# Optimization experiments

Hardware: AMD Instinct MI355X
Metric: run time of the kernel (lower is better)

The kernel has to match this reference:

```python
import jax, jax.numpy as jnp
import numpy as np

N = 8192
E = 262144
IN_F = 256
OUT_F = 64
H = 2
SLOPE = 0.2
NEG = -9e15


def _xavier(key, shape, gain):
    fan_in, fan_out = shape[-2], shape[-1]
    a = gain * np.sqrt(6.0 / (fan_in + fan_out))
    return jax.random.uniform(key, shape, jnp.float32, -a, a)


def setup_inputs() -> dict:
    key = jax.random.key(0)
    k_x, k_e, k_w, k_a1, k_a2 = jax.random.split(key, 5)
    gain = np.sqrt(2.0)
    return {
        "x": jax.random.normal(k_x, (N, IN_F), jnp.float32),
        "edge_index": jax.random.randint(k_e, (2, E), 0, N, jnp.int64),
        # per-head params (torch Linear stores weight [out,in]; we store [in,out])
        "W": _xavier(k_w, (H, IN_F, OUT_F), gain),
        "a1": _xavier(k_a1, (H, OUT_F), gain),
        "a2": _xavier(k_a2, (H, OUT_F), gain),
    }


def reference(x, edge_index, W, a1, a2):
    n = x.shape[0]
    # dense adjacency mask from COO edges (to_dense_adj: adj[src, dst] += 1; only adj>0 matters)
    adj = jnp.zeros((n, n), jnp.float32).at[edge_index[0], edge_index[1]].add(1.0)
    mask = adj > 0  # [N, N]

    xh = jnp.einsum('ni,hio->hno', x, W)          # [H, N, out]
    s1 = jnp.einsum('hno,ho->hn', xh, a1)          # a1(x): [H, N]
    s2 = jnp.einsum('hno,ho->hn', xh, a2)          # a2(x): [H, N]
    e = jnp.where(mask[None], s1[:, :, None] + s2[:, None, :], NEG)  # [H, N, N]
    e = jnp.where(e >= 0, e, SLOPE * e)            # leaky_relu
    att = jax.nn.softmax(e, axis=-1)               # [H, N, N]
    out = jnp.einsum('hnm,hmo->hno', att, xh)      # [H, N, out]
    # concat heads along feature dim (is_final_layer=False)
    return jnp.transpose(out, (1, 0, 2)).reshape(n, H * OUT_F)
```

## Files before the change

kernel.cpp:

```cpp
#include <hip/hip_runtime.h>

#define NN    8192
#define INF_  256
#define OUTF  64
#define NH    2
#define NE    262144
#define CAP   256
#define DEGS  16
#define SLOPE 0.2f

typedef __attribute__((ext_vector_type(8))) short short8;
typedef __attribute__((ext_vector_type(4))) float f32x4;
typedef __attribute__((ext_vector_type(2))) long long ll2;

__device__ __forceinline__ unsigned short f2bf(float f) {
  unsigned int u = __float_as_uint(f);
  u += 0x7fffu + ((u >> 16) & 1u);
  return (unsigned short)(u >> 16);
}

__global__ __launch_bounds__(256) void gemm_edge_kernel(
    const float* __restrict__ x, const int* __restrict__ ei,
    const float* __restrict__ W, const float* __restrict__ a1,
    const float* __restrict__ a2, int* __restrict__ deg,
    int* __restrict__ cols, float* __restrict__ xh,
    float2* __restrict__ s1v, float2* __restrict__ s2v) {
  const int b = blockIdx.x, t = threadIdx.x;

  __shared__ int s_nz;
  if (t == 0) s_nz = 0;
  __syncthreads();
  const int e0 = b * 512 + t * 2;
  if (((const unsigned int*)ei)[2 * e0 + 1] != 0u ||
      ((const unsigned int*)ei)[2 * e0 + 3] != 0u)
    s_nz = 1;
  __syncthreads();

  int i0, j0, i1, j1;
  if (s_nz == 0) {
    const ll2 a = *(const ll2*)((const long long*)ei + e0);
    const ll2 c = *(const ll2*)((const long long*)ei + NE + e0);
    i0 = (int)a[0]; i1 = (int)a[1]; j0 = (int)c[0]; j1 = (int)c[1];
  } else {
    const int2 a = *(const int2*)(ei + e0);
    const int2 c = *(const int2*)(ei + NE + e0);
    i0 = a.x; i1 = a.y; j0 = c.x; j1 = c.y;
  }
  const int p0 = atomicAdd(&deg[i0 * DEGS], 1);
  const int p1 = atomicAdd(&deg[i1 * DEGS], 1);

  const int l = t & 63, w = t >> 6;
  const int lo = l & 15, hi = l >> 4;
  const int n0 = b * 16;
  __shared__ float p1s[4][16], p2s[4][16];

  const int tc0 = w * 2, tc1 = w * 2 + 1;
  const int h0 = tc0 >> 2, h1 = tc1 >> 2;
  const int col0 = (tc0 * 16 + lo) & 63, col1 = (tc1 * 16 + lo) & 63;
  const float* wp0 = W + (size_t)h0 * (INF_ * OUTF) + (size_t)(hi * 8) * OUTF + col0;
  const float* wp1 = W + (size_t)h1 * (INF_ * OUTF) + (size_t)(hi * 8) * OUTF + col1;
  const float* xp = x + (size_t)(n0 + lo) * INF_ + hi * 8;

  f32x4 acc0 = {0.f, 0.f, 0.f, 0.f};
  f32x4 acc1 = {0.f, 0.f, 0.f, 0.f};

#define KSTEP(ks)                                                              \
  {                                                                            \
    const float4 f0 = *(const float4*)(xp + (ks) * 32);                        \
    const float4 f1 = *(const float4*)(xp + (ks) * 32 + 4);                    \
    short8 a_;                                                                 \
    a_[0] = (short)f2bf(f0.x); a_[1] = (short)f2bf(f0.y);                      \
    a_[2] = (short)f2bf(f0.z); a_[3] = (short)f2bf(f0.w);                      \
    a_[4] = (short)f2bf(f1.x); a_[5] = (short)f2bf(f1.y);                      \
    a_[6] = (short)f2bf(f1.z); a_[7] = (short)f2bf(f1.w);                      \
    const float* wq0 = wp0 + (size_t)(ks) * 32 * OUTF;                         \
    short8 b0_;                                                                \
    b0_[0] = (short)f2bf(wq0[0 * OUTF]); b0_[1] = (short)f2bf(wq0[1 * OUTF]);  \
    b0_[2] = (short)f2bf(wq0[2 * OUTF]); b0_[3] = (short)f2bf(wq0[3 * OUTF]);  \
    b0_[4] = (short)f2bf(wq0[4 * OUTF]); b0_[5] = (short)f2bf(wq0[5 * OUTF]);  \
    b0_[6] = (short)f2bf(wq0[6 * OUTF]); b0_[7] = (short)f2bf(wq0[7 * OUTF]);  \
    acc0 = __builtin_amdgcn_mfma_f32_16x16x32_bf16(a_, b0_, acc0, 0, 0, 0);    \
    const float* wq1 = wp1 + (size_t)(ks) * 32 * OUTF;                         \
    short8 b1_;                                                                \
    b1_[0] = (short)f2bf(wq1[0 * OUTF]); b1_[1] = (short)f2bf(wq1[1 * OUTF]);  \
    b1_[2] = (short)f2bf(wq1[2 * OUTF]); b1_[3] = (short)f2bf(wq1[3 * OUTF]);  \
    b1_[4] = (short)f2bf(wq1[4 * OUTF]); b1_[5] = (short)f2bf(wq1[5 * OUTF]);  \
    b1_[6] = (short)f2bf(wq1[6 * OUTF]); b1_[7] = (short)f2bf(wq1[7 * OUTF]);  \
    acc1 = __builtin_amdgcn_mfma_f32_16x16x32_bf16(a_, b1_, acc1, 0, 0, 0);    \
  }

  KSTEP(0) KSTEP(1) KSTEP(2) KSTEP(3) KSTEP(4) KSTEP(5) KSTEP(6) KSTEP(7)
#undef KSTEP

  if (p0 < CAP) cols[i0 * CAP + p0] = j0;
  if (p1 < CAP) cols[i1 * CAP + p1] = j1;

  {
    float* o0 = xh + ((size_t)h0 * NN + n0 + hi * 4) * OUTF + col0;
    float* o1 = xh + ((size_t)h1 * NN + n0 + hi * 4) * OUTF + col1;
    o0[0 * OUTF] = acc0[0]; o0[1 * OUTF] = acc0[1];
    o0[2 * OUTF] = acc0[2]; o0[3 * OUTF] = acc0[3];
    o1[0 * OUTF] = acc1[0]; o1[1 * OUTF] = acc1[1];
    o1[2 * OUTF] = acc1[2]; o1[3 * OUTF] = acc1[3];
  }
  const float a10 = a1[h0 * OUTF + col0], a11 = a1[h1 * OUTF + col1];
  const float a20 = a2[h0 * OUTF + col0], a21 = a2[h1 * OUTF + col1];
#pragma unroll
  for (int r = 0; r < 4; ++r) {
    float p1v = acc0[r] * a10 + acc1[r] * a11;
    float p2v = acc0[r] * a20 + acc1[r] * a21;
#pragma unroll
    for (int s = 1; s < 16; s <<= 1) {
      p1v += __shfl_xor(p1v, s, 64);
      p2v += __shfl_xor(p2v, s, 64);
    }
    if (lo == 0) {
      p1s[w][hi * 4 + r] = p1v;
      p2s[w][hi * 4 + r] = p2v;
    }
  }
  __syncthreads();
  if (t < 16) {
    float2 v1, v2;
    v1.x = p1s[0][t] + p1s[1][t];  v1.y = p1s[2][t] + p1s[3][t];
    v2.x = p2s[0][t] + p2s[1][t];  v2.y = p2s[2][t] + p2s[3][t];
    s1v[n0 + t] = v1;
    s2v[n0 + t] = v2;
  }
}

__global__ __launch_bounds__(128) void agg_kernel(const float* __restrict__ xh,
                                                  const float2* __restrict__ s1v,
                                                  const float2* __restrict__ s2v,
                                                  const int* __restrict__ deg,
                                                  const int* __restrict__ cols,
                                                  float* __restrict__ out) {
  const int i = blockIdx.x;
  const int t = threadIdx.x;
  const int h = t >> 6, lane = t & 63;
  __shared__ unsigned int bm[NN / 32];
  __shared__ unsigned long long vmask;
  __shared__ int   cjs[CAP];
  __shared__ float wts[NH][CAP];
  int d = deg[i * DEGS];
  if (d > CAP) d = CAP;
  bm[t] = 0u; bm[t + 128] = 0u;
  __syncthreads();

  const float* base = xh + (size_t)h * NN * OUTF;
  const int c4 = lane & 15, r = lane >> 4;

  if (d == 0) {
    f32x4 acc = {0.f, 0.f, 0.f, 0.f};
    for (int p = r; p < NN; p += 4)
      acc += *(const f32x4*)(base + (size_t)p * OUTF + 4 * c4);
#pragma unroll
    for (int c = 0; c < 4; ++c) {
      acc[c] += __shfl_xor(acc[c], 16, 64);
      acc[c] += __shfl_xor(acc[c], 32, 64);
    }
    if (lane < 16) {
      const float sc = 1.f / (float)NN;
      float4 o;
      o.x = acc[0] * sc; o.y = acc[1] * sc; o.z = acc[2] * sc; o.w = acc[3] * sc;
      *(float4*)(out + (size_t)i * (NH * OUTF) + h * OUTF + 4 * lane) = o;
    }
    return;
  }

  if (d <= 64) {
    int j = 0;
    const bool valid = lane < d;
    if (valid) j = cols[i * CAP + lane];
    if (h == 0) {
      bool dup = false;
      if (valid) {
        const unsigned int old = atomicOr(&bm[j >> 5], 1u << (j & 31));
        dup = (old >> (j & 31)) & 1u;
      }
      const unsigned long long bal = __ballot(valid && !dup);
      if (lane == 0) vmask = bal;
    }
    __syncthreads();
    const bool kp = (vmask >> lane) & 1ull;
    float sc = -1e30f;
    if (kp) {
      const float2 s1i2 = s1v[i];
      const float2 s2j2 = s2v[j];
      sc = (h ? s1i2.y : s1i2.x) + (h ? s2j2.y : s2j2.x);
      sc = (sc >= 0.f) ? sc : SLOPE * sc;
    }
    float m = sc;
#pragma unroll
    for (int s = 32; s > 0; s >>= 1) m = fmaxf(m, __shfl_xor(m, s, 64));
    const float wt = kp ? __expf(sc - m) : 0.f;
    float ds = wt;
#pragma unroll
    for (int s = 32; s > 0; s >>= 1) ds += __shfl_xor(ds, s, 64);
    const float inv = 1.f / ds;

    f32x4 acc = {0.f, 0.f, 0.f, 0.f};
#pragma unroll 2
    for (int p = 0; p < d; p += 4) {
      const int pr = p + r;
      float ww = __shfl(wt, pr, 64);
      int   jj = __shfl(j,  pr, 64);
      ww = (pr < d) ? ww : 0.f;
      jj = (ww > 0.f) ? jj : 0;
      acc += ww * *(const f32x4*)(base + (size_t)jj * OUTF + 4 * c4);
    }
#pragma unroll
    for (int c = 0; c < 4; ++c) {
      acc[c] += __shfl_xor(acc[c], 16, 64);
      acc[c] += __shfl_xor(acc[c], 32, 64);
    }
    if (lane < 16) {
      float4 o;
      o.x = acc[0] * inv; o.y = acc[1] * inv; o.z = acc[2] * inv; o.w = acc[3] * inv;
      *(float4*)(out + (size_t)i * (NH * OUTF) + h * OUTF + 4 * lane) = o;
    }
    return;
  }

  for (int p = t; p < d; p += 128) cjs[p] = cols[i * CAP + p];
  __syncthreads();
  if (h == 0) {
    for (int p = lane; p < d; p += 64) {
      const int j = cjs[p];
      const unsigned int old = atomicOr(&bm[j >> 5], 1u << (j & 31));
      if ((old >> (j & 31)) & 1u) cjs[p] = -1;
    }
  }
  __syncthreads();
  const float2 s1i2 = s1v[i];
  const float s1i = h ? s1i2.y : s1i2.x;
  float m = -1e30f;
  for (int p = lane; p < d; p += 64) {
    const int j = cjs[p];
    float sc = -1e30f;
    if (j >= 0) {
      const float2 s2j2 = s2v[j];
      sc = s1i + (h ? s2j2.y : s2j2.x);
      sc = (sc >= 0.f) ? sc : SLOPE * sc;
    }
    wts[h][p] = sc;
    m = fmaxf(m, sc);
  }
#pragma unroll
  for (int s = 32; s > 0; s >>= 1) m = fmaxf(m, __shfl_xor(m, s, 64));
  float ds = 0.f;
  for (int p = lane; p < d; p += 64) {
    const float sc = wts[h][p];
    const float w2 = (sc > -1e29f) ? __expf(sc - m) : 0.f;
    wts[h][p] = w2;
    ds += w2;
  }
#pragma unroll
  for (int s = 32; s > 0; s >>= 1) ds += __shfl_xor(ds, s, 64);
  const float inv = 1.f / ds;
  float acc = 0.f;
  for (int p = 0; p < d; ++p) {
    const float w2 = wts[h][p];
    if (w2 > 0.f) acc += w2 * base[(size_t)cjs[p] * OUTF + lane];
  }
  out[(size_t)i * (NH * OUTF) + h * OUTF + lane] = acc * inv;
}

extern "C" void kernel_launch(void* const* d_in, const int* in_sizes, int n_in,
                              void* d_out, int out_size, void* d_ws, size_t ws_size,
                              hipStream_t stream) {
  const float* x  = (const float*)d_in[0];
  const int*   ei = (const int*)d_in[1];
  const float* W  = (const float*)d_in[2];
  const float* a1 = (const float*)d_in[3];
  const float* a2 = (const float*)d_in[4];
  float* out = (float*)d_out;

  char* ws = (char*)d_ws;
  float*  xh   = (float*)(ws);
  float2* s1v  = (float2*)(ws + (4u << 20));
  float2* s2v  = (float2*)(ws + (4u << 20) + (64u << 10));
  int*    deg  = (int*)  (ws + (4u << 20) + (128u << 10));
  int*    cols = (int*)  (ws + (5u << 20));

  hipMemsetAsync(deg, 0, (size_t)NN * DEGS * 4, stream);
  gemm_edge_kernel<<<512, 256, 0, stream>>>(x, ei, W, a1, a2, deg, cols,
                                            xh, s1v, s2v);
  agg_kernel<<<NN, 128, 0, stream>>>(xh, s1v, s2v, deg, cols, out);
}
```

Baseline: 48.64 us.

## Split degree counters into four sub-buckets and separate edge blocks from GEMM blocks

Edge insertion now runs in its own 512 blocks, launched alongside the GEMM blocks instead of inside them. Each node's adjacency list is split into four sub-buckets of 64 slots, selected by edge index mod 4, which spreads atomic contention across four padded counters. The aggregation kernel reads the four counts, builds prefix offsets and remaps each slot index to its sub-bucket. This costs a 4x larger memset, extra branching in agg, and a lower per-bucket capacity that could drop edges when a bucket holds more than 64.

```diff
diff --git a/kernel.cpp b/kernel.cpp
--- a/kernel.cpp
+++ b/kernel.cpp
@@ -1,13 +1,15 @@
 #include <hip/hip_runtime.h>
 
-#define NN    8192
-#define INF_  256
-#define OUTF  64
-#define NH    2
-#define NE    262144
-#define CAP   256
-#define DEGS  16
-#define SLOPE 0.2f
+#define NN     8192
+#define INF_   256
+#define OUTF   64
+#define NH     2
+#define NE     262144
+#define CAP    256
+#define NSUB   4
+#define SUBCAP 64
+#define DEGS   16
+#define SLOPE  0.2f
 
 typedef __attribute__((ext_vector_type(8))) short short8;
 typedef __attribute__((ext_vector_type(4))) float f32x4;
@@ -27,27 +29,33 @@
     float2* __restrict__ s1v, float2* __restrict__ s2v) {
   const int b = blockIdx.x, t = threadIdx.x;
 
-  __shared__ int s_nz;
-  if (t == 0) s_nz = 0;
-  __syncthreads();
-  const int e0 = b * 512 + t * 2;
-  if (((const unsigned int*)ei)[2 * e0 + 1] != 0u ||
-      ((const unsigned int*)ei)[2 * e0 + 3] != 0u)
-    s_nz = 1;
-  __syncthreads();
-
-  int i0, j0, i1, j1;
-  if (s_nz == 0) {
-    const ll2 a = *(const ll2*)((const long long*)ei + e0);
-    const ll2 c = *(const ll2*)((const long long*)ei + NE + e0);
-    i0 = (int)a[0]; i1 = (int)a[1]; j0 = (int)c[0]; j1 = (int)c[1];
-  } else {
-    const int2 a = *(const int2*)(ei + e0);
-    const int2 c = *(const int2*)(ei + NE + e0);
-    i0 = a.x; i1 = a.y; j0 = c.x; j1 = c.y;
-  }
-  const int p0 = atomicAdd(&deg[i0 * DEGS], 1);
-  const int p1 = atomicAdd(&deg[i1 * DEGS], 1);
+  if (b >= 512) {
+    const int eb = b - 512;
+    const int e0 = eb * 512 + t * 2;
+    __shared__ int s_nz;
+    if (t == 0) s_nz = 0;
+    __syncthreads();
+    if (((const unsigned int*)ei)[2 * e0 + 1] != 0u ||
+        ((const unsigned int*)ei)[2 * e0 + 3] != 0u)
+      s_nz = 1;
+    __syncthreads();
+    int i0, j0, i1, j1;
+    if (s_nz == 0) {
+      const ll2 a = *(const ll2*)((const long long*)ei + e0);
+      const ll2 c = *(const ll2*)((const long long*)ei + NE + e0);
+      i0 = (int)a[0]; i1 = (int)a[1]; j0 = (int)c[0]; j1 = (int)c[1];
+    } else {
+      const int2 a = *(const int2*)(ei + e0);
+      const int2 c = *(const int2*)(ei + NE + e0);
+      i0 = a.x; i1 = a.y; j0 = c.x; j1 = c.y;
+    }
+    const int c0 = e0 & 3, c1 = (e0 + 1) & 3;
+    const int p0 = atomicAdd(&deg[(c0 * NN + i0) * DEGS], 1);
+    if (p0 < SUBCAP) cols[i0 * CAP + c0 * SUBCAP + p0] = j0;
+    const int p1 = atomicAdd(&deg[(c1 * NN + i1) * DEGS], 1);
+    if (p1 < SUBCAP) cols[i1 * CAP + c1 * SUBCAP + p1] = j1;
+    return;
+  }
 
   const int l = t & 63, w = t >> 6;
   const int lo = l & 15, hi = l >> 4;
@@ -92,9 +100,6 @@
   KSTEP(0) KSTEP(1) KSTEP(2) KSTEP(3) KSTEP(4) KSTEP(5) KSTEP(6) KSTEP(7)
 #undef KSTEP
 
-  if (p0 < CAP) cols[i0 * CAP + p0] = j0;
-  if (p1 < CAP) cols[i1 * CAP + p1] = j1;
-
   {
     float* o0 = xh + ((size_t)h0 * NN + n0 + hi * 4) * OUTF + col0;
     float* o1 = xh + ((size_t)h1 * NN + n0 + hi * 4) * OUTF + col1;
@@ -142,8 +147,16 @@
   __shared__ unsigned long long vmask;
   __shared__ int   cjs[CAP];
   __shared__ float wts[NH][CAP];
-  int d = deg[i * DEGS];
-  if (d > CAP) d = CAP;
+
+  int cnt0 = deg[(0 * NN + i) * DEGS];
+  int cnt1 = deg[(1 * NN + i) * DEGS];
+  int cnt2 = deg[(2 * NN + i) * DEGS];
+  int cnt3 = deg[(3 * NN + i) * DEGS];
+  cnt0 = min(cnt0, SUBCAP); cnt1 = min(cnt1, SUBCAP);
+  cnt2 = min(cnt2, SUBCAP); cnt3 = min(cnt3, SUBCAP);
+  const int P1 = cnt0, P2 = P1 + cnt1, P3 = P2 + cnt2;
+  const int d = __builtin_amdgcn_readfirstlane(P3 + cnt3);
+
   bm[t] = 0u; bm[t + 128] = 0u;
   __syncthreads();
 
@@ -171,7 +184,14 @@
   if (d <= 64) {
     int j = 0;
     const bool valid = lane < d;
-    if (valid) j = cols[i * CAP + lane];
+    if (valid) {
+      int cc, off;
+      if (lane < P1)      { cc = 0; off = lane; }
+      else if (lane < P2) { cc = 1; off = lane - P1; }
+      else if (lane < P3) { cc = 2; off = lane - P2; }
+      else                { cc = 3; off = lane - P3; }
+      j = cols[i * CAP + cc * SUBCAP + off];
+    }
     if (h == 0) {
       bool dup = false;
       if (valid) {
@@ -222,7 +242,14 @@
     return;
   }
 
-  for (int p = t; p < d; p += 128) cjs[p] = cols[i * CAP + p];
+  for (int p = t; p < d; p += 128) {
+    int cc, off;
+    if (p < P1)      { cc = 0; off = p; }
+    else if (p < P2) { cc = 1; off = p - P1; }
+    else if (p < P3) { cc = 2; off = p - P2; }
+    else             { cc = 3; off = p - P3; }
+    cjs[p] = cols[i * CAP + cc * SUBCAP + off];
+  }
   __syncthreads();
   if (h == 0) {
     for (int p = lane; p < d; p += 64) {
@@ -281,10 +308,10 @@
   float2* s1v  = (float2*)(ws + (4u << 20));
   float2* s2v  = (float2*)(ws + (4u << 20) + (64u << 10));
   int*    deg  = (int*)  (ws + (4u << 20) + (128u << 10));
-  int*    cols = (int*)  (ws + (5u << 20));
-
-  hipMemsetAsync(deg, 0, (size_t)NN * DEGS * 4, stream);
-  gemm_edge_kernel<<<512, 256, 0, stream>>>(x, ei, W, a1, a2, deg, cols,
-                                            xh, s1v, s2v);
+  int*    cols = (int*)  (ws + (7u << 20));
+
+  hipMemsetAsync(deg, 0, (size_t)NSUB * NN * DEGS * 4, stream);
+  gemm_edge_kernel<<<1024, 256, 0, stream>>>(x, ei, W, a1, a2, deg, cols,
+                                             xh, s1v, s2v);
   agg_kernel<<<NN, 128, 0, stream>>>(xh, s1v, s2v, deg, cols, out);
 }
```

Result: faster. 46.54 us (-4.3%).

## Replace CSR edge lists with dense adjacency bitmap and in-kernel compaction

Applied to the files above, without the earlier changes.

Edges are now recorded by atomicOr into a per-row 8192-bit bitmap, which replaces the per-row degree counters and column lists. The edge pass moves into separate blocks of the first kernel, so GEMM blocks no longer carry edge work. The aggregation kernel rebuilds a deduplicated, sorted neighbor list with popcount plus a wave prefix scan, which removes the shared-memory duplicate detection and the conditional branches. In exchange, an 8 MB bitmap must be zeroed by memset and read once per row, adding memory traffic compared with the old small degree and column arrays.

```diff
diff --git a/kernel.cpp b/kernel.cpp
--- a/kernel.cpp
+++ b/kernel.cpp
@@ -5,8 +5,7 @@
 #define OUTF  64
 #define NH    2
 #define NE    262144
-#define CAP   256
-#define DEGS  16
+#define NW    256
 #define SLOPE 0.2f
 
 typedef __attribute__((ext_vector_type(8))) short short8;
@@ -22,32 +21,35 @@
 __global__ __launch_bounds__(256) void gemm_edge_kernel(
     const float* __restrict__ x, const int* __restrict__ ei,
     const float* __restrict__ W, const float* __restrict__ a1,
-    const float* __restrict__ a2, int* __restrict__ deg,
-    int* __restrict__ cols, float* __restrict__ xh,
-    float2* __restrict__ s1v, float2* __restrict__ s2v) {
+    const float* __restrict__ a2, unsigned* __restrict__ bits,
+    float* __restrict__ xh, float2* __restrict__ s1v,
+    float2* __restrict__ s2v) {
   const int b = blockIdx.x, t = threadIdx.x;
 
-  __shared__ int s_nz;
-  if (t == 0) s_nz = 0;
-  __syncthreads();
-  const int e0 = b * 512 + t * 2;
-  if (((const unsigned int*)ei)[2 * e0 + 1] != 0u ||
-      ((const unsigned int*)ei)[2 * e0 + 3] != 0u)
-    s_nz = 1;
-  __syncthreads();
-
-  int i0, j0, i1, j1;
-  if (s_nz == 0) {
-    const ll2 a = *(const ll2*)((const long long*)ei + e0);
-    const ll2 c = *(const ll2*)((const long long*)ei + NE + e0);
-    i0 = (int)a[0]; i1 = (int)a[1]; j0 = (int)c[0]; j1 = (int)c[1];
-  } else {
-    const int2 a = *(const int2*)(ei + e0);
-    const int2 c = *(const int2*)(ei + NE + e0);
-    i0 = a.x; i1 = a.y; j0 = c.x; j1 = c.y;
-  }
-  const int p0 = atomicAdd(&deg[i0 * DEGS], 1);
-  const int p1 = atomicAdd(&deg[i1 * DEGS], 1);
+  if (b >= 512) {
+    const int eb = b - 512;
+    const int e0 = eb * 512 + t * 2;
+    __shared__ int s_nz;
+    if (t == 0) s_nz = 0;
+    __syncthreads();
+    if (((const unsigned int*)ei)[2 * e0 + 1] != 0u ||
+        ((const unsigned int*)ei)[2 * e0 + 3] != 0u)
+      s_nz = 1;
+    __syncthreads();
+    int i0, j0, i1, j1;
+    if (s_nz == 0) {
+      const ll2 a = *(const ll2*)((const long long*)ei + e0);
+      const ll2 c = *(const ll2*)((const long long*)ei + NE + e0);
+      i0 = (int)a[0]; i1 = (int)a[1]; j0 = (int)c[0]; j1 = (int)c[1];
+    } else {
+      const int2 a = *(const int2*)(ei + e0);
+      const int2 c = *(const int2*)(ei + NE + e0);
+      i0 = a.x; i1 = a.y; j0 = c.x; j1 = c.y;
+    }
+    atomicOr(&bits[(size_t)i0 * NW + (j0 >> 5)], 1u << (j0 & 31));
+    atomicOr(&bits[(size_t)i1 * NW + (j1 >> 5)], 1u << (j1 & 31));
+    return;
+  }
 
   const int l = t & 63, w = t >> 6;
   const int lo = l & 15, hi = l >> 4;
@@ -92,9 +94,6 @@
   KSTEP(0) KSTEP(1) KSTEP(2) KSTEP(3) KSTEP(4) KSTEP(5) KSTEP(6) KSTEP(7)
 #undef KSTEP
 
-  if (p0 < CAP) cols[i0 * CAP + p0] = j0;
-  if (p1 < CAP) cols[i1 * CAP + p1] = j1;
-
   {
     float* o0 = xh + ((size_t)h0 * NN + n0 + hi * 4) * OUTF + col0;
     float* o1 = xh + ((size_t)h1 * NN + n0 + hi * 4) * OUTF + col1;
@@ -132,19 +131,36 @@
 __global__ __launch_bounds__(128) void agg_kernel(const float* __restrict__ xh,
                                                   const float2* __restrict__ s1v,
                                                   const float2* __restrict__ s2v,
-                                                  const int* __restrict__ deg,
-                                                  const int* __restrict__ cols,
+                                                  const unsigned* __restrict__ bits,
                                                   float* __restrict__ out) {
   const int i = blockIdx.x;
   const int t = threadIdx.x;
   const int h = t >> 6, lane = t & 63;
-  __shared__ unsigned int bm[NN / 32];
-  __shared__ unsigned long long vmask;
-  __shared__ int   cjs[CAP];
-  __shared__ float wts[NH][CAP];
-  int d = deg[i * DEGS];
-  if (d > CAP) d = CAP;
-  bm[t] = 0u; bm[t + 128] = 0u;
+  __shared__ int   cjs[NH][256];
+  __shared__ float wts[NH][256];
+
+  const uint4 bv = *(const uint4*)(bits + (size_t)i * NW + lane * 4);
+  const int myc = __popc(bv.x) + __popc(bv.y) + __popc(bv.z) + __popc(bv.w);
+  int incl = myc;
+#pragma unroll
+  for (int s = 1; s < 64; s <<= 1) {
+    const int v = __shfl_up(incl, s, 64);
+    if (lane >= s) incl += v;
+  }
+  int pos = incl - myc;
+  const int dt = __shfl(incl, 63, 64);
+  const int d = __builtin_amdgcn_readfirstlane(dt > 256 ? 256 : dt);
+  {
+    unsigned wv; int bj;
+    wv = bv.x; bj = lane * 128;
+    while (wv) { const int bb = __ffs(wv) - 1; if (pos < 256) cjs[h][pos] = bj + bb; ++pos; wv &= wv - 1; }
+    wv = bv.y; bj = lane * 128 + 32;
+    while (wv) { const int bb = __ffs(wv) - 1; if (pos < 256) cjs[h][pos] = bj + bb; ++pos; wv &= wv - 1; }
+    wv = bv.z; bj = lane * 128 + 64;
+    while (wv) { const int bb = __ffs(wv) - 1; if (pos < 256) cjs[h][pos] = bj + bb; ++pos; wv &= wv - 1; }
+    wv = bv.w; bj = lane * 128 + 96;
+    while (wv) { const int bb = __ffs(wv) - 1; if (pos < 256) cjs[h][pos] = bj + bb; ++pos; wv &= wv - 1; }
+  }
   __syncthreads();
 
   const float* base = xh + (size_t)h * NN * OUTF;
@@ -169,20 +185,8 @@
   }
 
   if (d <= 64) {
-    int j = 0;
-    const bool valid = lane < d;
-    if (valid) j = cols[i * CAP + lane];
-    if (h == 0) {
-      bool dup = false;
-      if (valid) {
-        const unsigned int old = atomicOr(&bm[j >> 5], 1u << (j & 31));
-        dup = (old >> (j & 31)) & 1u;
-      }
-      const unsigned long long bal = __ballot(valid && !dup);
-      if (lane == 0) vmask = bal;
-    }
-    __syncthreads();
-    const bool kp = (vmask >> lane) & 1ull;
+    const bool kp = lane < d;
+    const int j = kp ? cjs[h][lane] : 0;
     float sc = -1e30f;
     if (kp) {
       const float2 s1i2 = s1v[i];
@@ -222,27 +226,13 @@
     return;
   }
 
-  for (int p = t; p < d; p += 128) cjs[p] = cols[i * CAP + p];
-  __syncthreads();
-  if (h == 0) {
-    for (int p = lane; p < d; p += 64) {
-      const int j = cjs[p];
-      const unsigned int old = atomicOr(&bm[j >> 5], 1u << (j & 31));
-      if ((old >> (j & 31)) & 1u) cjs[p] = -1;
-    }
-  }
-  __syncthreads();
   const float2 s1i2 = s1v[i];
   const float s1i = h ? s1i2.y : s1i2.x;
   float m = -1e30f;
   for (int p = lane; p < d; p += 64) {
-    const int j = cjs[p];
-    float sc = -1e30f;
-    if (j >= 0) {
-      const float2 s2j2 = s2v[j];
-      sc = s1i + (h ? s2j2.y : s2j2.x);
-      sc = (sc >= 0.f) ? sc : SLOPE * sc;
-    }
+    const float2 s2j2 = s2v[cjs[h][p]];
+    float sc = s1i + (h ? s2j2.y : s2j2.x);
+    sc = (sc >= 0.f) ? sc : SLOPE * sc;
     wts[h][p] = sc;
     m = fmaxf(m, sc);
   }
@@ -250,8 +240,7 @@
   for (int s = 32; s > 0; s >>= 1) m = fmaxf(m, __shfl_xor(m, s, 64));
   float ds = 0.f;
   for (int p = lane; p < d; p += 64) {
-    const float sc = wts[h][p];
-    const float w2 = (sc > -1e29f) ? __expf(sc - m) : 0.f;
+    const float w2 = __expf(wts[h][p] - m);
     wts[h][p] = w2;
     ds += w2;
   }
@@ -259,10 +248,8 @@
   for (int s = 32; s > 0; s >>= 1) ds += __shfl_xor(ds, s, 64);
   const float inv = 1.f / ds;
   float acc = 0.f;
-  for (int p = 0; p < d; ++p) {
-    const float w2 = wts[h][p];
-    if (w2 > 0.f) acc += w2 * base[(size_t)cjs[p] * OUTF + lane];
-  }
+  for (int p = 0; p < d; ++p)
+    acc += wts[h][p] * base[(size_t)cjs[h][p] * OUTF + lane];
   out[(size_t)i * (NH * OUTF) + h * OUTF + lane] = acc * inv;
 }
 
@@ -277,14 +264,13 @@
   float* out = (float*)d_out;
 
   char* ws = (char*)d_ws;
-  float*  xh   = (float*)(ws);
-  float2* s1v  = (float2*)(ws + (4u << 20));
-  float2* s2v  = (float2*)(ws + (4u << 20) + (64u << 10));
-  int*    deg  = (int*)  (ws + (4u << 20) + (128u << 10));
-  int*    cols = (int*)  (ws + (5u << 20));
-
-  hipMemsetAsync(deg, 0, (size_t)NN * DEGS * 4, stream);
-  gemm_edge_kernel<<<512, 256, 0, stream>>>(x, ei, W, a1, a2, deg, cols,
-                                            xh, s1v, s2v);
-  agg_kernel<<<NN, 128, 0, stream>>>(xh, s1v, s2v, deg, cols, out);
-}
+  unsigned* bits = (unsigned*)(ws);
+  float*    xh   = (float*)(ws + (8u << 20));
+  float2*   s1v  = (float2*)(ws + (12u << 20));
+  float2*   s2v  = (float2*)(ws + (12u << 20) + (64u << 10));
+
+  hipMemsetAsync(bits, 0, (size_t)NN * NW * 4, stream);
+  gemm_edge_kernel<<<1024, 256, 0, stream>>>(x, ei, W, a1, a2, bits,
+                                             xh, s1v, s2v);
+  agg_kernel<<<NN, 128, 0, stream>>>(xh, s1v, s2v, bits, out);
+}
```

After: 47.71 us. About the same (-1.9%).
